# Performance work log

Measured on AMD Instinct MI355X. Metric: run time of the kernel, lower is better.

The kernel has to match this reference:

```python
import jax, jax.numpy as jnp
import numpy as np

B, C, U = 8, 32, 32
K = 5            # powers = k + 1 with k = 4
N1, N2 = 256, 256


def setup_inputs() -> dict:
    key = jax.random.key(0)
    k_x, k_c1, k_c2, k_w = jax.random.split(key, 4)
    x = jax.random.normal(k_x, (B, C, N1, N2), dtype=jnp.float32)
    # Chebyshev polynomial bases T_0..T_k of the (rescaled) Laplacians of the
    # two factor graphs; registered buffers in the torch module.
    cheb1 = jax.random.normal(k_c1, (K, N1, N1), dtype=jnp.float32)
    cheb2 = jax.random.normal(k_c2, (K, N2, N2), dtype=jnp.float32)
    # Trainable anisotropic coefficients [powers, powers, channels, units],
    # initialized N(0, 0.001) in the original module.
    coefs = jax.random.normal(k_w, (K, K, C, U), dtype=jnp.float32) * 0.001
    return {"x": x, "cheb1": cheb1, "cheb2": cheb2, "coefs": coefs}


def reference(x, cheb1, cheb2, coefs):
    """Fused form of the anisotropic Chebyshev convolution.

    Original triple loop computes
      out[b,u,m,n] = sum_{k1,k2,i,p,q}
          coefs[k1,k2,i,u] * cheb1[k1,p,m] * cheb2[k2,q,n] * x[b,i,p,q]
    """
    # Filter along the first graph axis for every power k1: [B, K, C, N1, N2]
    a = jnp.einsum('kpm,bipq->bkimq', cheb1, x)
    # Contract channels and k1 with the learned coefficients: [B, K, U, N1, N2]
    c = jnp.einsum('bkimq,kliu->blumq', a, coefs)
    # Filter along the second graph axis for every power k2: [B, U, N1, N2]
    out = jnp.einsum('blumq,lqn->bumn', c, cheb2)
    return out
```

## Files before the change

kernel.cpp:

```cpp
#include <hip/hip_runtime.h>
#include <stdint.h>

#define WB 8
#define WC 32
#define WU 32
#define WK 5
#define WN 256
#define NN 65536
#define KC 160
#define KQ 1280

typedef __attribute__((ext_vector_type(8))) short bf8;
typedef __attribute__((ext_vector_type(8))) unsigned short us8;
typedef __attribute__((ext_vector_type(4))) float f4;

__device__ __forceinline__ unsigned short f2b(float f) {
    union { float f; uint32_t u; } v; v.f = f;
    uint32_t u = v.u;
    return (unsigned short)((u + 0x7FFFu + ((u >> 16) & 1u)) >> 16);
}

__device__ __forceinline__ void gload16(const unsigned short* g, unsigned short* l) {
    __builtin_amdgcn_global_load_lds(
        (const __attribute__((address_space(1))) unsigned int*)g,
        (__attribute__((address_space(3))) unsigned int*)l, 16, 0, 0);
}

__global__ void prep_small(const float* __restrict__ cheb1,
                           const float* __restrict__ cheb2,
                           const float* __restrict__ coefs,
                           unsigned short* __restrict__ c1T,
                           unsigned short* __restrict__ c2T,
                           unsigned short* __restrict__ WtP) {
    int idx = blockIdx.x * 256 + threadIdx.x;
    if (idx < WK * NN) {
        int k = idx / NN, r = idx % NN, m = r / WN, p = r % WN;
        c1T[idx] = f2b(cheb1[(k * WN + p) * WN + m]);
    }
    if (idx < WN * KQ) {
        int n = idx / KQ, r = idx % KQ;
        c2T[idx] = f2b(cheb2[r * WN + n]);
    }
    if (idx < KC * KC) {
        int e = idx & 7, lane = (idx >> 3) & 63, r = idx >> 9;
        int mf = r % 5, kk = (r / 5) % 5, mh = r / 25;
        int lu = mh * 80 + mf * 16 + (lane & 15);
        int ki = kk * 32 + (lane >> 4) * 8 + e;
        int l = lu >> 5, u = lu & 31, k = ki >> 5, i = ki & 31;
        WtP[idx] = f2b(coefs[((k * WK + l) * WC + i) * WU + u]);
    }
}

__global__ void prep_x(const float* __restrict__ x, unsigned short* __restrict__ xT) {
    __shared__ unsigned short tile[64][72];
    int bi = blockIdx.z;
    int p0 = blockIdx.y * 64, q0 = blockIdx.x * 64;
    const float* src = x + (size_t)bi * NN;
    unsigned short* dst = xT + (size_t)bi * NN;
    int t = threadIdx.x;
    int c4 = (t & 15) * 4, r0 = t >> 4;
    for (int it = 0; it < 4; ++it) {
        int r = r0 + it * 16;
        float4 v = *reinterpret_cast<const float4*>(&src[(size_t)(p0 + r) * WN + q0 + c4]);
        tile[r][c4 + 0] = f2b(v.x); tile[r][c4 + 1] = f2b(v.y);
        tile[r][c4 + 2] = f2b(v.z); tile[r][c4 + 3] = f2b(v.w);
    }
    __syncthreads();
    for (int it = 0; it < 4; ++it) {
        int q = r0 + it * 16;
        ushort4 o;
        o.x = tile[c4 + 0][q]; o.y = tile[c4 + 1][q];
        o.z = tile[c4 + 2][q]; o.w = tile[c4 + 3][q];
        *reinterpret_cast<ushort4*>(&dst[(size_t)(q0 + q) * WN + p0 + c4]) = o;
    }
}

__global__ __launch_bounds__(512, 4) void g1(const unsigned short* __restrict__ c1T,
                                             const unsigned short* __restrict__ xT,
                                             unsigned short* __restrict__ a, int b_base) {
    __shared__ unsigned short As[2][128 * 64];
    __shared__ unsigned short Bs[256 * 64];
    int p = blockIdx.x;
    int gpx = gridDim.x / 80;
    int xcd = p & 7, j = p >> 3;
    int grp = xcd * gpx + j / 10;
    int member = j % 10;
    int bl = grp >> 5, i = grp & 31;
    int row0 = member * 128;
    int b = b_base + bl;
    const unsigned short* Asrc = c1T;
    const unsigned short* Bsrc = xT + (size_t)(b * WC + i) * NN;
    unsigned short* Out = a + (size_t)bl * KC * NN;

    int t = threadIdx.x;
    int w = t >> 6, l = t & 63;
    int wm = (w >> 2) * 64, wn = (w & 3) * 64;
    int lr = l & 15, hi = l >> 4;
    int srow = l >> 3;
    int scol = ((l & 7) ^ srow) * 8;

    f4 acc[4][4];
    for (int mf = 0; mf < 4; ++mf) for (int nf = 0; nf < 4; ++nf) acc[mf][nf] = (f4)(0.0f);

#define G1_STAGE_A(buf, step) do { \
    int p0_ = (step) * 64; \
    for (int it = 0; it < 2; ++it) { \
        int chunk = it * 8 + w; int row = chunk * 8 + srow; \
        gload16(&Asrc[(size_t)(row0 + row) * 256 + p0_ + scol], &As[buf][chunk * 512]); } \
} while (0)
#define G1_STAGE_B(step) do { \
    int p0_ = (step) * 64; \
    for (int it = 0; it < 4; ++it) { \
        int chunk = it * 8 + w; int row = chunk * 8 + srow; \
        gload16(&Bsrc[(size_t)row * 256 + p0_ + scol], &Bs[chunk * 512]); } \
} while (0)

    G1_STAGE_A(0, 0);
    for (int step = 0; step < 4; ++step) {
        int cur = step & 1;
        G1_STAGE_B(step);
        if (step < 3) {
            G1_STAGE_A(cur ^ 1, step + 1);
            asm volatile("s_waitcnt vmcnt(2)" ::: "memory");
        } else {
            asm volatile("s_waitcnt vmcnt(0)" ::: "memory");
        }
        __builtin_amdgcn_s_barrier();
        asm volatile("" ::: "memory");
        for (int kk = 0; kk < 2; ++kk) {
            bf8 af[4], bfr[4];
            for (int mf = 0; mf < 4; ++mf) {
                int r = wm + mf * 16 + lr;
                af[mf] = *(const bf8*)&As[cur][r * 64 + (((kk * 4 + hi) ^ (r & 7)) * 8)];
            }
            for (int nf = 0; nf < 4; ++nf) {
                int rb = wn + nf * 16 + lr;
                bfr[nf] = *(const bf8*)&Bs[rb * 64 + (((kk * 4 + hi) ^ (rb & 7)) * 8)];
            }
            for (int mf = 0; mf < 4; ++mf)
                for (int nf = 0; nf < 4; ++nf)
                    acc[mf][nf] = __builtin_amdgcn_mfma_f32_16x16x32_bf16(af[mf], bfr[nf], acc[mf][nf], 0, 0, 0);
        }
        asm volatile("" ::: "memory");
        __builtin_amdgcn_s_barrier();
    }
#undef G1_STAGE_A
#undef G1_STAGE_B
    for (int mf = 0; mf < 4; ++mf)
        for (int nf = 0; nf < 4; ++nf)
            for (int j2 = 0; j2 < 4; ++j2) {
                int grow = row0 + wm + mf * 16 + hi * 4 + j2;
                int k = grow >> 8, m = grow & 255;
                int q = wn + nf * 16 + lr;
                Out[(size_t)(k * 32 + i) * NN + m * 256 + q] = f2b(acc[mf][nf][j2]);
            }
}

__global__ __launch_bounds__(512, 4) void g2p(const unsigned short* __restrict__ WtP,
                                              const unsigned short* __restrict__ a,
                                              unsigned short* __restrict__ c) {
    __shared__ unsigned short Bt[128 * 172];
    int bl = blockIdx.y;
    int n0 = blockIdx.x * 128;
    const unsigned short* asrc = a + (size_t)bl * KC * NN;
    unsigned short* Out = c + (size_t)bl * KC * NN;
    int t = threadIdx.x;

    for (int s = 0; s < 2; ++s) {
        int task = t + s * 512;
        if (task < 640) {
            int oct = task & 15, kq = task >> 4;
            const unsigned short* src = asrc + (size_t)(kq * 4) * NN + n0 + oct * 8;
            us8 v0 = *(const us8*)&src[0 * NN];
            us8 v1 = *(const us8*)&src[1 * NN];
            us8 v2 = *(const us8*)&src[2 * NN];
            us8 v3 = *(const us8*)&src[3 * NN];
            #pragma unroll
            for (int j = 0; j < 8; ++j) {
                ushort4 wv;
                wv.x = v0[j]; wv.y = v1[j]; wv.z = v2[j]; wv.w = v3[j];
                *reinterpret_cast<ushort4*>(&Bt[(oct * 8 + j) * 172 + kq * 4]) = wv;
            }
        }
    }
    __syncthreads();

    int w = t >> 6, l = t & 63;
    int mh = w >> 2, nq = w & 3;
    int lr = l & 15, hi = l >> 4;
    f4 acc[5][2];
    for (int mf = 0; mf < 5; ++mf) { acc[mf][0] = (f4)(0.0f); acc[mf][1] = (f4)(0.0f); }

    for (int kk = 0; kk < 5; ++kk) {
        int k0 = kk * 32 + hi * 8;
        bf8 bfr[2];
        #pragma unroll
        for (int nf = 0; nf < 2; ++nf) {
            int pix = (nq * 2 + nf) * 16 + lr;
            typedef __attribute__((ext_vector_type(4))) short s4v;
            s4v lo  = *(const s4v*)&Bt[pix * 172 + k0];
            s4v hi4 = *(const s4v*)&Bt[pix * 172 + k0 + 4];
            bfr[nf] = __builtin_shufflevector(lo, hi4, 0, 1, 2, 3, 4, 5, 6, 7);
        }
        #pragma unroll
        for (int mf = 0; mf < 5; ++mf) {
            bf8 afr = *(const bf8*)&WtP[(size_t)((((mh * 5 + kk) * 5 + mf) << 6) + l) * 8];
            acc[mf][0] = __builtin_amdgcn_mfma_f32_16x16x32_bf16(afr, bfr[0], acc[mf][0], 0, 0, 0);
            acc[mf][1] = __builtin_amdgcn_mfma_f32_16x16x32_bf16(afr, bfr[1], acc[mf][1], 0, 0, 0);
        }
    }
    for (int mf = 0; mf < 5; ++mf)
        for (int nf = 0; nf < 2; ++nf)
            for (int j = 0; j < 4; ++j) {
                int row = mh * 80 + mf * 16 + hi * 4 + j;
                int col = n0 + (nq * 2 + nf) * 16 + lr;
                Out[(size_t)row * NN + col] = f2b(acc[mf][nf][j]);
            }
}

__global__ __launch_bounds__(512, 1) void g3(const unsigned short* __restrict__ c,
                                             const unsigned short* __restrict__ c2T,
                                             float* __restrict__ out, int b_base) {
    __shared__ unsigned short As[2][256 * 64];
    __shared__ unsigned short Bs[2][256 * 64];
    int bl = blockIdx.y;
    int b = b_base + bl;
    int u = blockIdx.x;
    const unsigned short* Csrc = c + (size_t)bl * KC * NN;

    int t_ = threadIdx.x;
    int w = t_ >> 6, l = t_ & 63;
    int wm = (w >> 2) * 128, wn = (w & 3) * 64;
    int lr = l & 15, hi = l >> 4;
    int srow = l >> 3;
    int scol = ((l & 7) ^ srow) * 8;

    f4 acc[8][4];
    for (int mf = 0; mf < 8; ++mf) for (int nf = 0; nf < 4; ++nf) acc[mf][nf] = (f4)(0.0f);

#define ST_A(s, h, kt) do { \
    int lq_ = (kt) >> 2, q0_ = ((kt) & 3) * 64; \
    const unsigned short* base = Csrc + (size_t)(lq_ * 32 + u) * NN + q0_; \
    for (int it = 0; it < 2; ++it) { \
        int chunk = it * 8 + w; int row = (h) * 128 + chunk * 8 + srow; \
        gload16(&base[(size_t)row * 256 + scol], &As[s][(h) * 8192 + chunk * 512]); } \
} while (0)
#define ST_B(s, h, kt) do { \
    const unsigned short* base = c2T + (size_t)((h) * 128) * KQ + (kt) * 64; \
    for (int it = 0; it < 2; ++it) { \
        int chunk = it * 8 + w; int rrow = chunk * 8 + srow; \
        gload16(&base[(size_t)rrow * KQ + scol], &Bs[s][(h) * 8192 + chunk * 512]); } \
} while (0)

    ST_A(0, 0, 0); ST_A(0, 1, 0); ST_B(0, 0, 0); ST_B(0, 1, 0);

    for (int t = 0; t < 20; ++t) {
        int s = t & 1;
        asm volatile("s_waitcnt vmcnt(0)" ::: "memory");
        __builtin_amdgcn_s_barrier();
        asm volatile("" ::: "memory");
        const unsigned short* A = As[s];
        const unsigned short* B = Bs[s];
        bf8 af[8], b0, b1;
        if (t < 19) ST_A(s ^ 1, 0, t + 1);
        #pragma unroll
        for (int mf = 0; mf < 8; ++mf) {
            int r = wm + mf * 16 + lr;
            af[mf] = *(const bf8*)&A[r * 64 + ((hi ^ (r & 7)) * 8)];
        }
        { int rb = wn + lr;      b0 = *(const bf8*)&B[rb * 64 + ((hi ^ (rb & 7)) * 8)];
          rb = wn + 16 + lr;     b1 = *(const bf8*)&B[rb * 64 + ((hi ^ (rb & 7)) * 8)]; }
        __builtin_amdgcn_s_setprio(1);
        #pragma unroll
        for (int mf = 0; mf < 8; ++mf) {
            acc[mf][0] = __builtin_amdgcn_mfma_f32_16x16x32_bf16(af[mf], b0, acc[mf][0], 0, 0, 0);
            acc[mf][1] = __builtin_amdgcn_mfma_f32_16x16x32_bf16(af[mf], b1, acc[mf][1], 0, 0, 0);
        }
        __builtin_amdgcn_s_setprio(0);
        if (t < 19) ST_A(s ^ 1, 1, t + 1);
        { int rb = wn + 32 + lr; b0 = *(const bf8*)&B[rb * 64 + ((hi ^ (rb & 7)) * 8)];
          rb = wn + 48 + lr;     b1 = *(const bf8*)&B[rb * 64 + ((hi ^ (rb & 7)) * 8)]; }
        __builtin_amdgcn_s_setprio(1);
        #pragma unroll
        for (int mf = 0; mf < 8; ++mf) {
            acc[mf][2] = __builtin_amdgcn_mfma_f32_16x16x32_bf16(af[mf], b0, acc[mf][2], 0, 0, 0);
            acc[mf][3] = __builtin_amdgcn_mfma_f32_16x16x32_bf16(af[mf], b1, acc[mf][3], 0, 0, 0);
        }
        __builtin_amdgcn_s_setprio(0);
        if (t < 19) ST_B(s ^ 1, 0, t + 1);
        #pragma unroll
        for (int mf = 0; mf < 8; ++mf) {
            int r = wm + mf * 16 + lr;
            af[mf] = *(const bf8*)&A[r * 64 + (((4 + hi) ^ (r & 7)) * 8)];
        }
        { int rb = wn + lr;      b0 = *(const bf8*)&B[rb * 64 + (((4 + hi) ^ (rb & 7)) * 8)];
          rb = wn + 16 + lr;     b1 = *(const bf8*)&B[rb * 64 + (((4 + hi) ^ (rb & 7)) * 8)]; }
        __builtin_amdgcn_s_setprio(1);
        #pragma unroll
        for (int mf = 0; mf < 8; ++mf) {
            acc[mf][0] = __builtin_amdgcn_mfma_f32_16x16x32_bf16(af[mf], b0, acc[mf][0], 0, 0, 0);
            acc[mf][1] = __builtin_amdgcn_mfma_f32_16x16x32_bf16(af[mf], b1, acc[mf][1], 0, 0, 0);
        }
        __builtin_amdgcn_s_setprio(0);
        if (t < 19) ST_B(s ^ 1, 1, t + 1);
        { int rb = wn + 32 + lr; b0 = *(const bf8*)&B[rb * 64 + (((4 + hi) ^ (rb & 7)) * 8)];
          rb = wn + 48 + lr;     b1 = *(const bf8*)&B[rb * 64 + (((4 + hi) ^ (rb & 7)) * 8)]; }
        __builtin_amdgcn_s_setprio(1);
        #pragma unroll
        for (int mf = 0; mf < 8; ++mf) {
            acc[mf][2] = __builtin_amdgcn_mfma_f32_16x16x32_bf16(af[mf], b0, acc[mf][2], 0, 0, 0);
            acc[mf][3] = __builtin_amdgcn_mfma_f32_16x16x32_bf16(af[mf], b1, acc[mf][3], 0, 0, 0);
        }
        __builtin_amdgcn_s_setprio(0);
        asm volatile("" ::: "memory");
    }
#undef ST_A
#undef ST_B
    for (int mf = 0; mf < 8; ++mf)
        for (int nf = 0; nf < 4; ++nf)
            for (int j = 0; j < 4; ++j) {
                int m = wm + mf * 16 + hi * 4 + j;
                int n = wn + nf * 16 + lr;
                out[((size_t)(b * WU + u) * WN + m) * WN + n] = acc[mf][nf][j];
            }
}

extern "C" void kernel_launch(void* const* d_in, const int* in_sizes, int n_in,
                              void* d_out, int out_size, void* d_ws, size_t ws_size,
                              hipStream_t stream) {
    const float* x     = (const float*)d_in[0];
    const float* cheb1 = (const float*)d_in[1];
    const float* cheb2 = (const float*)d_in[2];
    const float* coefs = (const float*)d_in[3];
    float* out = (float*)d_out;
    unsigned short* ws = (unsigned short*)d_ws;

    size_t off = 0;
    unsigned short* xT  = ws + off; off += (size_t)WB * WC * NN;
    unsigned short* c1T = ws + off; off += (size_t)WK * NN;
    unsigned short* c2T = ws + off; off += (size_t)WN * KQ;
    unsigned short* WtP = ws + off; off += (size_t)KC * KC;
    size_t fixed_elems = off;
    size_t a1 = (size_t)KC * NN;

    prep_small<<<1280, 256, 0, stream>>>(cheb1, cheb2, coefs, c1T, c2T, WtP);
    prep_x<<<dim3(4, 4, WB * WC), 256, 0, stream>>>(x, xT);

    size_t avail = ws_size / 2;
    size_t rem = avail > fixed_elems ? avail - fixed_elems : 0;

    if (rem >= 9 * a1) {
        int nb = (int)((rem - 8 * a1) / a1);
        if (nb < 1) nb = 1;
        if (nb > WB) nb = WB;
        unsigned short* a_ = ws + fixed_elems;
        unsigned short* c_ = a_ + (size_t)nb * a1;
        for (int b0 = 0; b0 < WB; b0 += nb) {
            int cur = (WB - b0 < nb) ? (WB - b0) : nb;
            g1<<<dim3(cur * 320), 512, 0, stream>>>(c1T, xT, a_, b0);
            g2p<<<dim3(512, cur), 512, 0, stream>>>(WtP, a_, c_ + (size_t)b0 * a1);
        }
        g3<<<dim3(32, WB), 512, 0, stream>>>(c_, c2T, out, 0);
    } else {
        size_t per_b = 2 * a1;
        int nb = (int)(rem / per_b);
        if (nb < 1) nb = 1;
        if (nb > WB) nb = WB;
        unsigned short* a_ = ws + fixed_elems;
        unsigned short* c_ = a_ + (size_t)nb * a1;
        for (int b0 = 0; b0 < WB; b0 += nb) {
            int cur = (WB - b0 < nb) ? (WB - b0) : nb;
            g1<<<dim3(cur * 320), 512, 0, stream>>>(c1T, xT, a_, b0);
            g2p<<<dim3(512, cur), 512, 0, stream>>>(WtP, a_, c_);
            g3<<<dim3(32, cur), 512, 0, stream>>>(c_, c2T, out, b0);
        }
    }
}
```

Baseline: 269.9 us.

## Merge prep kernels and restructure g3 pipeline with split waits

Folds the two preprocessing kernels into a single launch of 4096 blocks, so one launch handles the x transpose and the small casts. In g3, each stage's A and B halves are now issued together, and the first barrier waits only on vmcnt(4) instead of draining all loads. Waves that read the second M or N half wait again before computing, and a trailing barrier protects buffer reuse. Both half-K MFMA blocks now load all four B fragments at once. The aim is to overlap global-to-LDS loads with MFMA work and save a launch, at the cost of an extra barrier per iteration and more live registers.

```diff
diff --git a/kernel.cpp b/kernel.cpp
--- a/kernel.cpp
+++ b/kernel.cpp
@@ -26,13 +26,19 @@
         (__attribute__((address_space(3))) unsigned int*)l, 16, 0, 0);
 }
 
-__global__ void prep_small(const float* __restrict__ cheb1,
-                           const float* __restrict__ cheb2,
-                           const float* __restrict__ coefs,
-                           unsigned short* __restrict__ c1T,
-                           unsigned short* __restrict__ c2T,
-                           unsigned short* __restrict__ WtP) {
-    int idx = blockIdx.x * 256 + threadIdx.x;
+__global__ void prep_all(const float* __restrict__ x,
+                         const float* __restrict__ cheb1,
+                         const float* __restrict__ cheb2,
+                         const float* __restrict__ coefs,
+                         unsigned short* __restrict__ xT,
+                         unsigned short* __restrict__ c1T,
+                         unsigned short* __restrict__ c2T,
+                         unsigned short* __restrict__ WtP) {
+    __shared__ unsigned short tile[64][72];
+    int blk = blockIdx.x;
+    int t = threadIdx.x;
+
+    int idx = blk * 256 + t;
     if (idx < WK * NN) {
         int k = idx / NN, r = idx % NN, m = r / WN, p = r % WN;
         c1T[idx] = f2b(cheb1[(k * WN + p) * WN + m]);
@@ -49,15 +55,11 @@
         int l = lu >> 5, u = lu & 31, k = ki >> 5, i = ki & 31;
         WtP[idx] = f2b(coefs[((k * WK + l) * WC + i) * WU + u]);
     }
-}
-
-__global__ void prep_x(const float* __restrict__ x, unsigned short* __restrict__ xT) {
-    __shared__ unsigned short tile[64][72];
-    int bi = blockIdx.z;
-    int p0 = blockIdx.y * 64, q0 = blockIdx.x * 64;
+
+    int bx = blk & 3, by = (blk >> 2) & 3, bi = blk >> 4;
+    int p0 = by * 64, q0 = bx * 64;
     const float* src = x + (size_t)bi * NN;
     unsigned short* dst = xT + (size_t)bi * NN;
-    int t = threadIdx.x;
     int c4 = (t & 15) * 4, r0 = t >> 4;
     for (int it = 0; it < 4; ++it) {
         int r = r0 + it * 16;
@@ -230,10 +232,13 @@
 
     int t_ = threadIdx.x;
     int w = t_ >> 6, l = t_ & 63;
-    int wm = (w >> 2) * 128, wn = (w & 3) * 64;
+    int wmh = w >> 2;
+    int wn = (w & 3) * 64;
+    int bnh = (w & 3) >> 1;
     int lr = l & 15, hi = l >> 4;
     int srow = l >> 3;
     int scol = ((l & 7) ^ srow) * 8;
+    int late = wmh | bnh;
 
     f4 acc[8][4];
     for (int mf = 0; mf < 8; ++mf) for (int nf = 0; nf < 4; ++nf) acc[mf][nf] = (f4)(0.0f);
@@ -252,74 +257,70 @@
         gload16(&base[(size_t)rrow * KQ + scol], &Bs[s][(h) * 8192 + chunk * 512]); } \
 } while (0)
 
-    ST_A(0, 0, 0); ST_A(0, 1, 0); ST_B(0, 0, 0); ST_B(0, 1, 0);
+    ST_A(0, 0, 0); ST_B(0, 0, 0); ST_A(0, 1, 0); ST_B(0, 1, 0);
 
     for (int t = 0; t < 20; ++t) {
         int s = t & 1;
-        asm volatile("s_waitcnt vmcnt(0)" ::: "memory");
+        asm volatile("s_waitcnt vmcnt(4)" ::: "memory");
         __builtin_amdgcn_s_barrier();
         asm volatile("" ::: "memory");
+        if (t < 19) { ST_A(s ^ 1, 0, t + 1); ST_B(s ^ 1, 0, t + 1); }
+        if (late) {
+            if (t < 19) asm volatile("s_waitcnt vmcnt(4)" ::: "memory");
+            else        asm volatile("s_waitcnt vmcnt(0)" ::: "memory");
+        }
         const unsigned short* A = As[s];
         const unsigned short* B = Bs[s];
-        bf8 af[8], b0, b1;
-        if (t < 19) ST_A(s ^ 1, 0, t + 1);
-        #pragma unroll
-        for (int mf = 0; mf < 8; ++mf) {
-            int r = wm + mf * 16 + lr;
-            af[mf] = *(const bf8*)&A[r * 64 + ((hi ^ (r & 7)) * 8)];
-        }
-        { int rb = wn + lr;      b0 = *(const bf8*)&B[rb * 64 + ((hi ^ (rb & 7)) * 8)];
-          rb = wn + 16 + lr;     b1 = *(const bf8*)&B[rb * 64 + ((hi ^ (rb & 7)) * 8)]; }
-        __builtin_amdgcn_s_setprio(1);
-        #pragma unroll
-        for (int mf = 0; mf < 8; ++mf) {
-            acc[mf][0] = __builtin_amdgcn_mfma_f32_16x16x32_bf16(af[mf], b0, acc[mf][0], 0, 0, 0);
-            acc[mf][1] = __builtin_amdgcn_mfma_f32_16x16x32_bf16(af[mf], b1, acc[mf][1], 0, 0, 0);
-        }
-        __builtin_amdgcn_s_setprio(0);
-        if (t < 19) ST_A(s ^ 1, 1, t + 1);
-        { int rb = wn + 32 + lr; b0 = *(const bf8*)&B[rb * 64 + ((hi ^ (rb & 7)) * 8)];
-          rb = wn + 48 + lr;     b1 = *(const bf8*)&B[rb * 64 + ((hi ^ (rb & 7)) * 8)]; }
-        __builtin_amdgcn_s_setprio(1);
-        #pragma unroll
-        for (int mf = 0; mf < 8; ++mf) {
-            acc[mf][2] = __builtin_amdgcn_mfma_f32_16x16x32_bf16(af[mf], b0, acc[mf][2], 0, 0, 0);
-            acc[mf][3] = __builtin_amdgcn_mfma_f32_16x16x32_bf16(af[mf], b1, acc[mf][3], 0, 0, 0);
-        }
-        __builtin_amdgcn_s_setprio(0);
-        if (t < 19) ST_B(s ^ 1, 0, t + 1);
-        #pragma unroll
-        for (int mf = 0; mf < 8; ++mf) {
-            int r = wm + mf * 16 + lr;
-            af[mf] = *(const bf8*)&A[r * 64 + (((4 + hi) ^ (r & 7)) * 8)];
-        }
-        { int rb = wn + lr;      b0 = *(const bf8*)&B[rb * 64 + (((4 + hi) ^ (rb & 7)) * 8)];
-          rb = wn + 16 + lr;     b1 = *(const bf8*)&B[rb * 64 + (((4 + hi) ^ (rb & 7)) * 8)]; }
-        __builtin_amdgcn_s_setprio(1);
-        #pragma unroll
-        for (int mf = 0; mf < 8; ++mf) {
-            acc[mf][0] = __builtin_amdgcn_mfma_f32_16x16x32_bf16(af[mf], b0, acc[mf][0], 0, 0, 0);
-            acc[mf][1] = __builtin_amdgcn_mfma_f32_16x16x32_bf16(af[mf], b1, acc[mf][1], 0, 0, 0);
-        }
-        __builtin_amdgcn_s_setprio(0);
-        if (t < 19) ST_B(s ^ 1, 1, t + 1);
-        { int rb = wn + 32 + lr; b0 = *(const bf8*)&B[rb * 64 + (((4 + hi) ^ (rb & 7)) * 8)];
-          rb = wn + 48 + lr;     b1 = *(const bf8*)&B[rb * 64 + (((4 + hi) ^ (rb & 7)) * 8)]; }
-        __builtin_amdgcn_s_setprio(1);
-        #pragma unroll
-        for (int mf = 0; mf < 8; ++mf) {
-            acc[mf][2] = __builtin_amdgcn_mfma_f32_16x16x32_bf16(af[mf], b0, acc[mf][2], 0, 0, 0);
-            acc[mf][3] = __builtin_amdgcn_mfma_f32_16x16x32_bf16(af[mf], b1, acc[mf][3], 0, 0, 0);
-        }
-        __builtin_amdgcn_s_setprio(0);
+        {
+            bf8 af[8], bfr[4];
+            #pragma unroll
+            for (int mf = 0; mf < 8; ++mf) {
+                int r = wmh * 128 + mf * 16 + lr;
+                af[mf] = *(const bf8*)&A[r * 64 + ((hi ^ (r & 7)) * 8)];
+            }
+            #pragma unroll
+            for (int nf = 0; nf < 4; ++nf) {
+                int rb = wn + nf * 16 + lr;
+                bfr[nf] = *(const bf8*)&B[rb * 64 + ((hi ^ (rb & 7)) * 8)];
+            }
+            __builtin_amdgcn_s_setprio(1);
+            #pragma unroll
+            for (int mf = 0; mf < 8; ++mf)
+                #pragma unroll
+                for (int nf = 0; nf < 4; ++nf)
+                    acc[mf][nf] = __builtin_amdgcn_mfma_f32_16x16x32_bf16(af[mf], bfr[nf], acc[mf][nf], 0, 0, 0);
+            __builtin_amdgcn_s_setprio(0);
+        }
+        if (t < 19) { ST_A(s ^ 1, 1, t + 1); ST_B(s ^ 1, 1, t + 1); }
+        {
+            bf8 af[8], bfr[4];
+            #pragma unroll
+            for (int mf = 0; mf < 8; ++mf) {
+                int r = wmh * 128 + mf * 16 + lr;
+                af[mf] = *(const bf8*)&A[r * 64 + (((4 + hi) ^ (r & 7)) * 8)];
+            }
+            #pragma unroll
+            for (int nf = 0; nf < 4; ++nf) {
+                int rb = wn + nf * 16 + lr;
+                bfr[nf] = *(const bf8*)&B[rb * 64 + (((4 + hi) ^ (rb & 7)) * 8)];
+            }
+            __builtin_amdgcn_s_setprio(1);
+            #pragma unroll
+            for (int mf = 0; mf < 8; ++mf)
+                #pragma unroll
+                for (int nf = 0; nf < 4; ++nf)
+                    acc[mf][nf] = __builtin_amdgcn_mfma_f32_16x16x32_bf16(af[mf], bfr[nf], acc[mf][nf], 0, 0, 0);
+            __builtin_amdgcn_s_setprio(0);
+        }
         asm volatile("" ::: "memory");
+        __builtin_amdgcn_s_barrier();
     }
 #undef ST_A
 #undef ST_B
     for (int mf = 0; mf < 8; ++mf)
         for (int nf = 0; nf < 4; ++nf)
             for (int j = 0; j < 4; ++j) {
-                int m = wm + mf * 16 + hi * 4 + j;
+                int m = wmh * 128 + mf * 16 + hi * 4 + j;
                 int n = wn + nf * 16 + lr;
                 out[((size_t)(b * WU + u) * WN + m) * WN + n] = acc[mf][nf][j];
             }
@@ -343,8 +344,7 @@
     size_t fixed_elems = off;
     size_t a1 = (size_t)KC * NN;
 
-    prep_small<<<1280, 256, 0, stream>>>(cheb1, cheb2, coefs, c1T, c2T, WtP);
-    prep_x<<<dim3(4, 4, WB * WC), 256, 0, stream>>>(x, xT);
+    prep_all<<<4096, 256, 0, stream>>>(x, cheb1, cheb2, coefs, xT, c1T, c2T, WtP);
 
     size_t avail = ws_size / 2;
     size_t rem = avail > fixed_elems ? avail - fixed_elems : 0;
```

Measured after the change: 268.2 us. No clear change (-0.6%).
